# Kernel optimization log

Measured on AMD Instinct MI355X. Metric: run time of the kernel, lower is better.

The kernel has to match this reference:

```python
import jax, jax.numpy as jnp
import numpy as np

FEATURES = 4096
BATCH = 2048


def setup_inputs() -> dict:
    key = jax.random.key(0)
    kx, kk = jax.random.split(key)
    x = jax.random.normal(kx, (BATCH, FEATURES), dtype=jnp.float32)
    kernel = jax.random.normal(kk, (FEATURES,), dtype=jnp.float32)
    return {"x": x, "kernel": kernel}


def reference(x, kernel):
    n = kernel.shape[0]
    i = jnp.arange(n)[:, None]   # [n,1]
    j = jnp.arange(n)[None, :]   # [1,n]
    idx = i - j                   # Toeplitz offsets
    # W[i,j] = kernel[i-j] if i>=j else 0  (causal lower-triangular Toeplitz)
    W = jnp.where(idx >= 0, kernel[jnp.clip(idx, 0, n - 1)], 0.0)
    # out[b,i] = sum_{j<=i} x[b,j] * kernel[i-j]  == x @ W.T
    return x @ W.T
```

## Files before the change

### kernel.cpp

```cpp
#include <hip/hip_runtime.h>
#include <hip/hip_bf16.h>


typedef unsigned short u16;
typedef __attribute__((ext_vector_type(8))) short  bf16x8;
typedef __attribute__((ext_vector_type(8))) unsigned short u16x8;
typedef __attribute__((ext_vector_type(4))) float  f32x4;

#define KDIM 4096
#define NDIM 4096
#define MDIM 2048
#define KREV_STRIDE 4608
#define KREV_BYTES  (8 * KREV_STRIDE * 2)
#define BSTRIDE 456
#define BBUF    (8 * BSTRIDE)

#define MFMA_BF16 __builtin_amdgcn_mfma_f32_16x16x32_bf16

static __device__ inline u16 f2bf(float f) {
  unsigned u = __builtin_bit_cast(unsigned, f);
  unsigned r = u + 0x7FFFu + ((u >> 16) & 1u);
  return (u16)(r >> 16);
}

static __device__ inline void async_copy16(const void* g, void* l) {
  __builtin_amdgcn_global_load_lds((const __attribute__((address_space(1))) void*)g,
                                   (__attribute__((address_space(3))) void*)l,
                                   16, 0, 0);
}

__global__ __launch_bounds__(256) void prep(const float* __restrict__ x,
                                            const float* __restrict__ kern,
                                            u16* __restrict__ xb,
                                            u16* __restrict__ krevs,
                                            int conv_blocks) {
  int kblk = (int)blockIdx.x - conv_blocks;
  if (kblk >= 0) {
    int u = kblk * 256 + threadIdx.x;
    for (int a = 0; a < 8; ++a) {
      int t = u + a - 8;
      u16 v = 0;
      if (t >= 0 && t <= 4095) v = f2bf(kern[4095 - t]);
      krevs[a * KREV_STRIDE + u] = v;
    }
  } else {
    unsigned tg  = blockIdx.x * 256 + threadIdx.x;
    unsigned l   = tg & 63;
    unsigned kb  = (tg >> 6) & 127;
    unsigned rg  = tg >> 13;
    unsigned row = rg * 16 + (l & 15);
    unsigned k   = kb * 32 + (l >> 4) * 8;
    const f32x4* p = (const f32x4*)(x + (size_t)row * KDIM + k);
    f32x4 v0 = p[0], v1 = p[1];
    u16x8 r;
    r[0] = f2bf(v0[0]); r[1] = f2bf(v0[1]); r[2] = f2bf(v0[2]); r[3] = f2bf(v0[3]);
    r[4] = f2bf(v1[0]); r[5] = f2bf(v1[1]); r[6] = f2bf(v1[2]); r[7] = f2bf(v1[3]);
    *(u16x8*)(xb + (size_t)tg * 8) = r;
  }
}

template <bool CONV>
__global__ __launch_bounds__(512, 4) void toeplitz_gemm(const void* __restrict__ Av,
                                                        const u16* __restrict__ krevs,
                                                        float* __restrict__ out) {
  __shared__ __align__(16) char smem_raw[36864];
  u16*   B_all = (u16*)smem_raw;
  f32x4* ep    = (f32x4*)smem_raw;

  const int tid  = threadIdx.x;
  const int w    = tid >> 6;
  const int g    = w >> 2;
  const int wl   = w & 3;
  const int lane = tid & 63;
  const int lane16 = lane & 15;
  const int quad   = lane >> 4;
  const int wm = wl >> 1;
  const int wn = wl & 1;

  const int b  = (int)blockIdx.x;
  const int x_ = b & 7;
  const int jj = b >> 3;
  const int q  = jj & 31;
  const int h2 = jj >> 5;
  const int mt = x_ + 8 * (q & 1);
  const int ct = h2 ? (q >> 1) : 31 - (q >> 1);
  const int n0 = ct * 128;
  const int m0 = mt * 128;
  const int W  = 3968 - n0;
  const int cmax = ct >> 1;

  int boff[4];
  for (int fn = 0; fn < 4; ++fn) {
    int n_g = n0 + wn * 64 + fn * 16 + lane16;
    int s0  = 4095 - n_g + quad * 8;
    int a   = s0 & 7;
    boff[fn] = a * BSTRIDE + (s0 - a + 8 - W);
  }

  f32x4 acc[4][4] = {};

  const int wmu = __builtin_amdgcn_readfirstlane(wm);
  const int gu  = __builtin_amdgcn_readfirstlane(g);
  const u16*   xb2 = (const u16*)Av;
  const float* xf  = (const float*)Av;
  int aoffs[4];
  for (int fm = 0; fm < 4; ++fm)
    aoffs[fm] = (mt * 8 + wmu * 4 + fm) * 65536 + gu * 1024 + lane * 8;
  const int rowb = m0 + wm * 64 + lane16;

  auto ldA = [&](int fm, int t, int kk) -> bf16x8 {
    return *(const bf16x8*)(xb2 + aoffs[fm] + t * 2048 + kk * 512);
  };
  auto ldAc = [&](int fm, int t, int kk) -> bf16x8 {
    const float* px = xf + (size_t)(rowb + fm * 16) * KDIM +
                      t * 128 + gu * 64 + kk * 32 + quad * 8;
    f32x4 v0 = *(const f32x4*)px, v1 = *(const f32x4*)(px + 4);
    u16x8 r;
    r[0]=f2bf(v0[0]); r[1]=f2bf(v0[1]); r[2]=f2bf(v0[2]); r[3]=f2bf(v0[3]);
    r[4]=f2bf(v1[0]); r[5]=f2bf(v1[1]); r[6]=f2bf(v1[2]); r[7]=f2bf(v1[3]);
    return __builtin_bit_cast(bf16x8, r);
  };
  auto stageB = [&](int c) {
    if (lane < 56)
      async_copy16(krevs + w * KREV_STRIDE + W + c * 256 + (lane << 3),
                   &B_all[(c & 1) * BBUF + w * BSTRIDE]);
  };

  if constexpr (!CONV) {
    bf16x8 afA[4], afB[4];
    stageB(0);
#pragma unroll
    for (int fm = 0; fm < 4; ++fm) afA[fm] = ldA(fm, 0, 0);
#pragma unroll
    for (int fm = 0; fm < 4; ++fm) afB[fm] = ldA(fm, 0, 1);
    asm volatile("s_waitcnt vmcnt(8)" ::: "memory");
    __builtin_amdgcn_s_barrier();
    asm volatile("" ::: "memory");

    for (int t = 0; ; ++t) {
      const u16* Bb  = B_all + ((t >> 1) & 1) * BBUF;
      const int  ksl = (t & 1) * 128 + g * 64;
#pragma unroll
      for (int fn = 0; fn < 4; ++fn) {
        bf16x8 bv = *(const bf16x8*)(&Bb[boff[fn] + ksl]);
#pragma unroll
        for (int fm = 0; fm < 4; ++fm)
          acc[fm][fn] = MFMA_BF16(afA[fm], bv, acc[fm][fn], 0, 0, 0);
      }
      if (t < ct)
#pragma unroll
        for (int fm = 0; fm < 4; ++fm) afA[fm] = ldA(fm, t + 1, 0);
      if (!(t & 1) && (t >> 1) + 1 <= cmax) stageB((t >> 1) + 1);
#pragma unroll
      for (int fn = 0; fn < 4; ++fn) {
        bf16x8 bv = *(const bf16x8*)(&Bb[boff[fn] + ksl + 32]);
#pragma unroll
        for (int fm = 0; fm < 4; ++fm)
          acc[fm][fn] = MFMA_BF16(afB[fm], bv, acc[fm][fn], 0, 0, 0);
      }
      if (t < ct)
#pragma unroll
        for (int fm = 0; fm < 4; ++fm) afB[fm] = ldA(fm, t + 1, 1);
      if (t == ct) break;
      if (t & 1) {
        asm volatile("s_waitcnt vmcnt(12)" ::: "memory");
        __builtin_amdgcn_s_barrier();
        asm volatile("" ::: "memory");
      }
    }
  } else {
    stageB(0);
    asm volatile("s_waitcnt vmcnt(0)" ::: "memory");
    __syncthreads();
    for (int t = 0; ; ++t) {
      const u16* Bb  = B_all + ((t >> 1) & 1) * BBUF;
      const int  ksl = (t & 1) * 128 + g * 64;
      if (!(t & 1) && (t >> 1) + 1 <= cmax) stageB((t >> 1) + 1);
#pragma unroll
      for (int kk = 0; kk < 2; ++kk) {
        bf16x8 af[4];
#pragma unroll
        for (int fm = 0; fm < 4; ++fm) af[fm] = ldAc(fm, t, kk);
#pragma unroll
        for (int fn = 0; fn < 4; ++fn) {
          bf16x8 bv = *(const bf16x8*)(&Bb[boff[fn] + ksl + kk * 32]);
#pragma unroll
          for (int fm = 0; fm < 4; ++fm)
            acc[fm][fn] = MFMA_BF16(af[fm], bv, acc[fm][fn], 0, 0, 0);
        }
      }
      if (t == ct) break;
      if (t & 1) {
        asm volatile("s_waitcnt vmcnt(0)" ::: "memory");
        __syncthreads();
      }
    }
  }

  const int j = tid & 255;
  for (int r = 0; r < 2; ++r) {
    __syncthreads();
    if (g == 1) {
      for (int fm2 = 0; fm2 < 2; ++fm2)
        for (int fn = 0; fn < 4; ++fn)
          ep[j * 9 + fm2 * 4 + fn] = acc[r * 2 + fm2][fn];
    }
    __syncthreads();
    if (g == 0) {
      for (int fm2 = 0; fm2 < 2; ++fm2)
        for (int fn = 0; fn < 4; ++fn)
          acc[r * 2 + fm2][fn] += ep[j * 9 + fm2 * 4 + fn];
    }
  }

  if (g == 0) {
    for (int fm = 0; fm < 4; ++fm) {
      int row_base = m0 + wm * 64 + fm * 16 + quad * 4;
      for (int fn = 0; fn < 4; ++fn) {
        int col = n0 + wn * 64 + fn * 16 + lane16;
        for (int r = 0; r < 4; ++r)
          out[(size_t)(row_base + r) * NDIM + col] = acc[fm][fn][r];
      }
    }
  }
}

extern "C" void kernel_launch(void* const* d_in, const int* in_sizes, int n_in,
                              void* d_out, int out_size, void* d_ws, size_t ws_size,
                              hipStream_t stream) {
  const float* x    = (const float*)d_in[0];
  const float* kern = (const float*)d_in[1];
  float* out = (float*)d_out;

  u16* krevs = (u16*)d_ws;
  u16* xb    = (u16*)((char*)d_ws + KREV_BYTES);
  const size_t need_fast = (size_t)KREV_BYTES + (size_t)MDIM * KDIM * 2;

  if (ws_size >= need_fast) {
    prep<<<4096 + 18, 256, 0, stream>>>(x, kern, xb, krevs, 4096);
    toeplitz_gemm<false><<<512, 512, 0, stream>>>(xb, krevs, out);
  } else {
    prep<<<18, 256, 0, stream>>>(x, kern, xb, krevs, 0);
    toeplitz_gemm<true><<<512, 512, 0, stream>>>(x, krevs, out);
  }
}
```

Measured before the change: 122.2 us.

## Preload full reversed-kernel band into LDS once and drop per-chunk barriers

Replaces the double-buffered per-chunk staging of the reversed Toeplitz kernel with a single upfront async copy of the whole band each block needs, with per-block stride sized to its causal tile count. This removes the main-loop barriers and B-staging waits so the loop only streams A fragments and issues MFMAs. In exchange, shared memory per block grows to about 67KB, which cuts how many blocks fit per CU, and the full upfront load sits on the critical path before any compute starts.

```diff
diff --git a/kernel.cpp b/kernel.cpp
--- a/kernel.cpp
+++ b/kernel.cpp
@@ -12,8 +12,6 @@
 #define MDIM 2048
 #define KREV_STRIDE 4608
 #define KREV_BYTES  (8 * KREV_STRIDE * 2)
-#define BSTRIDE 456
-#define BBUF    (8 * BSTRIDE)
 
 #define MFMA_BF16 __builtin_amdgcn_mfma_f32_16x16x32_bf16
 
@@ -63,7 +61,7 @@
 __global__ __launch_bounds__(512, 4) void toeplitz_gemm(const void* __restrict__ Av,
                                                         const u16* __restrict__ krevs,
                                                         float* __restrict__ out) {
-  __shared__ __align__(16) char smem_raw[36864];
+  __shared__ __align__(16) char smem_raw[68736];
   u16*   B_all = (u16*)smem_raw;
   f32x4* ep    = (f32x4*)smem_raw;
 
@@ -87,14 +85,16 @@
   const int n0 = ct * 128;
   const int m0 = mt * 128;
   const int W  = 3968 - n0;
-  const int cmax = ct >> 1;
+
+  const int LEN_e    = 128 * (ct + 1) + 160;
+  const int stride_e = 128 * (ct + 1) + 200;
 
   int boff[4];
   for (int fn = 0; fn < 4; ++fn) {
     int n_g = n0 + wn * 64 + fn * 16 + lane16;
     int s0  = 4095 - n_g + quad * 8;
     int a   = s0 & 7;
-    boff[fn] = a * BSTRIDE + (s0 - a + 8 - W);
+    boff[fn] = a * stride_e + (s0 - a + 8 - W);
   }
 
   f32x4 acc[4][4] = {};
@@ -120,29 +120,31 @@
     r[4]=f2bf(v1[0]); r[5]=f2bf(v1[1]); r[6]=f2bf(v1[2]); r[7]=f2bf(v1[3]);
     return __builtin_bit_cast(bf16x8, r);
   };
-  auto stageB = [&](int c) {
-    if (lane < 56)
-      async_copy16(krevs + w * KREV_STRIDE + W + c * 256 + (lane << 3),
-                   &B_all[(c & 1) * BBUF + w * BSTRIDE]);
-  };
+
+  {
+    const u16* src = krevs + w * KREV_STRIDE + W;
+    char* dstb = smem_raw + (size_t)w * stride_e * 2;
+    for (int c = 0; c * 512 < LEN_e; ++c) {
+      int idx = c * 512 + lane * 8;
+      if (idx < LEN_e)
+        async_copy16(src + idx, dstb + (size_t)c * 1024);
+    }
+  }
+  asm volatile("s_waitcnt vmcnt(0)" ::: "memory");
+  __builtin_amdgcn_s_barrier();
+  asm volatile("" ::: "memory");
 
   if constexpr (!CONV) {
     bf16x8 afA[4], afB[4];
-    stageB(0);
 #pragma unroll
     for (int fm = 0; fm < 4; ++fm) afA[fm] = ldA(fm, 0, 0);
 #pragma unroll
     for (int fm = 0; fm < 4; ++fm) afB[fm] = ldA(fm, 0, 1);
-    asm volatile("s_waitcnt vmcnt(8)" ::: "memory");
-    __builtin_amdgcn_s_barrier();
-    asm volatile("" ::: "memory");
-
     for (int t = 0; ; ++t) {
-      const u16* Bb  = B_all + ((t >> 1) & 1) * BBUF;
-      const int  ksl = (t & 1) * 128 + g * 64;
+      const int ks = t * 128 + g * 64;
 #pragma unroll
       for (int fn = 0; fn < 4; ++fn) {
-        bf16x8 bv = *(const bf16x8*)(&Bb[boff[fn] + ksl]);
+        bf16x8 bv = *(const bf16x8*)(&B_all[boff[fn] + ks]);
 #pragma unroll
         for (int fm = 0; fm < 4; ++fm)
           acc[fm][fn] = MFMA_BF16(afA[fm], bv, acc[fm][fn], 0, 0, 0);
@@ -150,32 +152,20 @@
       if (t < ct)
 #pragma unroll
         for (int fm = 0; fm < 4; ++fm) afA[fm] = ldA(fm, t + 1, 0);
-      if (!(t & 1) && (t >> 1) + 1 <= cmax) stageB((t >> 1) + 1);
 #pragma unroll
       for (int fn = 0; fn < 4; ++fn) {
-        bf16x8 bv = *(const bf16x8*)(&Bb[boff[fn] + ksl + 32]);
+        bf16x8 bv = *(const bf16x8*)(&B_all[boff[fn] + ks + 32]);
 #pragma unroll
         for (int fm = 0; fm < 4; ++fm)
           acc[fm][fn] = MFMA_BF16(afB[fm], bv, acc[fm][fn], 0, 0, 0);
       }
-      if (t < ct)
-#pragma unroll
-        for (int fm = 0; fm < 4; ++fm) afB[fm] = ldA(fm, t + 1, 1);
       if (t == ct) break;
-      if (t & 1) {
-        asm volatile("s_waitcnt vmcnt(12)" ::: "memory");
-        __builtin_amdgcn_s_barrier();
-        asm volatile("" ::: "memory");
-      }
+#pragma unroll
+      for (int fm = 0; fm < 4; ++fm) afB[fm] = ldA(fm, t + 1, 1);
     }
   } else {
-    stageB(0);
-    asm volatile("s_waitcnt vmcnt(0)" ::: "memory");
-    __syncthreads();
-    for (int t = 0; ; ++t) {
-      const u16* Bb  = B_all + ((t >> 1) & 1) * BBUF;
-      const int  ksl = (t & 1) * 128 + g * 64;
-      if (!(t & 1) && (t >> 1) + 1 <= cmax) stageB((t >> 1) + 1);
+    for (int t = 0; t <= ct; ++t) {
+      const int ks = t * 128 + g * 64;
 #pragma unroll
       for (int kk = 0; kk < 2; ++kk) {
         bf16x8 af[4];
@@ -183,16 +173,11 @@
         for (int fm = 0; fm < 4; ++fm) af[fm] = ldAc(fm, t, kk);
 #pragma unroll
         for (int fn = 0; fn < 4; ++fn) {
-          bf16x8 bv = *(const bf16x8*)(&Bb[boff[fn] + ksl + kk * 32]);
+          bf16x8 bv = *(const bf16x8*)(&B_all[boff[fn] + ks + kk * 32]);
 #pragma unroll
           for (int fm = 0; fm < 4; ++fm)
             acc[fm][fn] = MFMA_BF16(af[fm], bv, acc[fm][fn], 0, 0, 0);
         }
-      }
-      if (t == ct) break;
-      if (t & 1) {
-        asm volatile("s_waitcnt vmcnt(0)" ::: "memory");
-        __syncthreads();
       }
     }
   }
```

Result: faster. 117.0 us (-4.2%).
